# Kernel tuning notes

Hardware: AMD Instinct MI355X
Metric: run time of the kernel (lower is better)

Reference implementation:

```python
import jax, jax.numpy as jnp
import numpy as np

RATIO, NH, NG, KS, RF, UP = 4, 2, 2, 3, 11.0, 2


def _cln(t, g, b):
    # channel-wise LayerNorm on NCHW (LayerNormProxy), eps=1e-5
    mu = t.mean(axis=1, keepdims=True)
    var = ((t - mu) ** 2).mean(axis=1, keepdims=True)
    return (t - mu) * jax.lax.rsqrt(var + 1e-5) * g[None, :, None, None] + b[None, :, None, None]


def _resize_ac(img, oH, oW):
    # bilinear resize, align_corners=True (F.interpolate)
    H, W = img.shape[-2], img.shape[-1]
    ys = jnp.arange(oH, dtype=img.dtype) * ((H - 1) / (oH - 1))
    y0 = jnp.clip(jnp.floor(ys), 0, H - 2).astype(jnp.int32)
    wy = ys - y0.astype(img.dtype)
    xs = jnp.arange(oW, dtype=img.dtype) * ((W - 1) / (oW - 1))
    x0 = jnp.clip(jnp.floor(xs), 0, W - 2).astype(jnp.int32)
    wx = xs - x0.astype(img.dtype)
    t = img[..., y0, :] * (1.0 - wy)[:, None] + img[..., y0 + 1, :] * wy[:, None]
    return t[..., x0] * (1.0 - wx) + t[..., x0 + 1] * wx


def _grid_sample(img, iy, ix):
    # bilinear grid_sample, padding_mode='zeros', align_corners=True
    # img [Bg,Cx,H,W]; iy,ix [Bg,N] unnormalized input-pixel coords
    H, W = img.shape[-2], img.shape[-1]
    def one(im, yy, xx):
        y0f, x0f = jnp.floor(yy), jnp.floor(xx)
        wy, wx = yy - y0f, xx - x0f
        y0, x0 = y0f.astype(jnp.int32), x0f.astype(jnp.int32)
        def gat(yi, xi):
            valid = ((yi >= 0) & (yi < H) & (xi >= 0) & (xi < W)).astype(im.dtype)
            return im[:, jnp.clip(yi, 0, H - 1), jnp.clip(xi, 0, W - 1)] * valid[None]
        return (gat(y0, x0) * ((1 - wy) * (1 - wx))[None]
                + gat(y0, x0 + 1) * ((1 - wy) * wx)[None]
                + gat(y0 + 1, x0) * (wy * (1 - wx))[None]
                + gat(y0 + 1, x0 + 1) * (wy * wx)[None])
    return jax.vmap(one)(img, iy, ix)


def _conv2d(x, w, groups=1):
    return jax.lax.conv_general_dilated(x, w, (1, 1), 'SAME', feature_group_count=groups,
                                        dimension_numbers=('NCHW', 'OIHW', 'NCHW'))


def _forward(x, ln_g, ln_b, Wq, Wk, dw_w, off_ln_g, off_ln_b, off_w, off_b, rpb):
    B, C, H, W = x.shape
    hidden = C // RATIO
    gc = hidden // NG
    c2 = hidden // NH          # attn_dim per head
    oH, oW = int(H * UP), int(W * UP)
    N1, n = oH * oW, KS * KS
    scale = c2 ** -0.5
    v = x
    xn = _cln(x, ln_g, ln_b)
    q = jnp.einsum('oc,bchw->bohw', Wq, xn)
    k = jnp.einsum('oc,bchw->bohw', Wk, xn)
    q = _resize_ac(q, oH, oW)                        # [B,hidden,oH,oW]
    # offset prediction
    q_off = q.reshape(B * NG, gc, oH, oW)
    t = _conv2d(q_off, dw_w, groups=gc)
    t = _cln(t, off_ln_g, off_ln_b)
    t = jax.nn.gelu(t, approximate=False)
    pred = _conv2d(t, off_w) + off_b[None, :, None, None]  # [Bg,2*ks^2,oH,oW]
    pad = (KS - 1) // 2
    rng = jnp.arange(-pad, pad + 1, dtype=x.dtype)
    base = jnp.stack(jnp.meshgrid(rng, rng, indexing='ij'), axis=-1)  # [KS,KS,2] (y,x)
    off = jnp.tanh(pred).reshape(B * NG, KS, KS, 2, oH, oW) * RF + base[None, :, :, :, None, None]
    py = off[:, :, :, 0] + jnp.arange(oH, dtype=x.dtype)[None, None, None, :, None]
    px = off[:, :, :, 1] + jnp.arange(oW, dtype=x.dtype)[None, None, None, None, :]
    # normalize over (oH-1,oW-1) then denormalize onto (H-1,W-1) input grid (align_corners)
    iy = (py * ((H - 1) / (oH - 1))).reshape(B * NG, -1)
    ix = (px * ((W - 1) / (oW - 1))).reshape(B * NG, -1)
    kg = k.reshape(B * NG, hidden // NG, H, W)
    vg = v.reshape(B * NG, C // NG, H, W)
    kf = _grid_sample(kg, iy, ix).reshape(B, NG, hidden // NG, n, oH, oW)
    vf = _grid_sample(vg, iy, ix).reshape(B, NG, C // NG, n, oH, oW)
    # -> [B, N1, n, g*c] -> [B, nh, N1, n, c]
    kf = kf.transpose(0, 4, 5, 3, 1, 2).reshape(B, N1, n, NH, hidden // NH).transpose(0, 3, 1, 2, 4)
    vf = vf.transpose(0, 4, 5, 3, 1, 2).reshape(B, N1, n, NH, C // NH).transpose(0, 3, 1, 2, 4)
    kf = kf + rpb                                     # relative position bias on K
    qh = q.reshape(B, NH, c2, N1).transpose(0, 1, 3, 2) * scale  # [B,nh,N1,c2]
    attn = jax.nn.softmax(jnp.einsum('bhnc,bhnkc->bhnk', qh, kf), axis=-1)
    out = jnp.einsum('bhnk,bhnkc->bhnc', attn, vf)    # [B,nh,N1,C/nh]
    return out.transpose(0, 1, 3, 2).reshape(B, C, oH, oW)


def setup_inputs() -> dict:
    key = jax.random.key(0)
    ks = jax.random.split(key, 8)
    B, C, H, W = 2, 256, 48, 48
    hidden = C // RATIO
    gc = hidden // NG
    c2 = hidden // NH
    f32 = jnp.float32
    return {
        'x': jax.random.normal(ks[0], (B, C, H, W), f32),
        'ln_g': jnp.ones((C,), f32),
        'ln_b': jnp.zeros((C,), f32),
        'Wq': jax.random.normal(ks[1], (hidden, C), f32) * 0.05,
        'Wk': jax.random.normal(ks[2], (hidden, C), f32) * 0.05,
        'dw_w': jax.random.normal(ks[3], (gc, 1, 3, 3), f32) * 0.1,
        'off_ln_g': jnp.ones((gc,), f32),
        'off_ln_b': jnp.zeros((gc,), f32),
        'off_w': jax.random.normal(ks[4], (2 * KS * KS, gc, 3, 3), f32) * 0.02,
        'off_b': jnp.zeros((2 * KS * KS,), f32),
        'rpb': jax.random.normal(ks[5], (1, NH, 1, KS * KS, c2), f32) * 0.02,
    }


def reference(x, ln_g, ln_b, Wq, Wk, dw_w, off_ln_g, off_ln_b, off_w, off_b, rpb):
    return _forward(x, ln_g, ln_b, Wq, Wk, dw_w, off_ln_g, off_ln_b, off_w, off_b, rpb)
```

## Files before the change

### kernel.cpp

```cpp
#include <hip/hip_runtime.h>
#include <cstdint>
#include <cmath>

#define NB 2
#define NC 256
#define HW 2304
#define HID 64
#define OH 96
#define OW 96
#define N1 9216
#define SCALE_ATTN 0.17677669529663689f
#define RESZ ((float)(47.0/95.0))

__device__ __host__ inline int ocb_of(int w) { return w < 2 ? w * 5 : 10 + (w - 2) * 4; }
__device__ __host__ inline int cnt_of(int w) { return w < 2 ? 5 : 4; }

__global__ void kA_prep(const float* __restrict__ Wq, const float* __restrict__ Wk,
                        const float* __restrict__ off_w, const float* __restrict__ dw_w,
                        const float* __restrict__ off_b,
                        float* __restrict__ WT4, float* __restrict__ dwT,
                        float* __restrict__ wg, float* __restrict__ bsg) {
    int idx = blockIdx.x * 256 + threadIdx.x;
    if (idx < 256 * 128) {
        int c = idx >> 7, t = idx & 127;
        float v = (t < 64) ? Wq[t * 256 + c] : Wk[(t - 64) * 256 + c];
        WT4[(((size_t)(c >> 2) * 128) + t) * 4 + (c & 3)] = v;
    } else if (idx < 256 * 128 + 288) {
        int i = idx - 256 * 128;
        int wi = i >> 5, c = i & 31;
        dwT[i] = dw_w[c * 9 + wi];
    } else if (idx < 256 * 128 + 288 + 4 * 288 * 5) {
        int i = idx - (256 * 128 + 288);
        int w = i / 1440, r = i - w * 1440;
        int kk = r / 5, j = r - kk * 5;
        wg[i] = (j < cnt_of(w)) ? off_w[(ocb_of(w) + j) * 288 + kk] : 0.f;
    } else if (idx < 256 * 128 + 288 + 4 * 288 * 5 + 20) {
        int i = idx - (256 * 128 + 288 + 4 * 288 * 5);
        int w = i / 5, j = i - w * 5;
        bsg[i] = (j < cnt_of(w)) ? off_b[ocb_of(w) + j] : 0.f;
    }
}

__global__ __launch_bounds__(256) void k1_ln_qk(const float* __restrict__ x,
                         const float* __restrict__ ln_g, const float* __restrict__ ln_b,
                         const float* __restrict__ WT4,
                         float* __restrict__ q_pix, float* __restrict__ k_nhwc) {
    int blk = blockIdx.x;
    int tid = threadIdx.x;
    int wv = tid >> 6, lane = tid & 63;
    __shared__ float xs[4][256];
    {
        int pix = blk * 4 + wv;
        int b = pix / HW, p = pix - b * HW;
        const float* xb = x + (size_t)b * NC * HW + p;
        float v0 = xb[(size_t)lane * HW];
        float v1 = xb[(size_t)(lane + 64) * HW];
        float v2 = xb[(size_t)(lane + 128) * HW];
        float v3 = xb[(size_t)(lane + 192) * HW];
        float s = v0 + v1 + v2 + v3;
#pragma unroll
        for (int off = 1; off < 64; off <<= 1) s += __shfl_xor(s, off);
        float mu = s * (1.f / 256.f);
        float d0 = v0 - mu, d1 = v1 - mu, d2 = v2 - mu, d3 = v3 - mu;
        float q = d0 * d0 + d1 * d1 + d2 * d2 + d3 * d3;
#pragma unroll
        for (int off = 1; off < 64; off <<= 1) q += __shfl_xor(q, off);
        float rs = rsqrtf(q * (1.f / 256.f) + 1e-5f);
        xs[wv][lane]       = d0 * rs * ln_g[lane]       + ln_b[lane];
        xs[wv][lane + 64]  = d1 * rs * ln_g[lane + 64]  + ln_b[lane + 64];
        xs[wv][lane + 128] = d2 * rs * ln_g[lane + 128] + ln_b[lane + 128];
        xs[wv][lane + 192] = d3 * rs * ln_g[lane + 192] + ln_b[lane + 192];
    }
    __syncthreads();
    int o = tid & 127, ph = tid >> 7;
    float a0 = 0.f, a1 = 0.f;
    const float4* wp = (const float4*)WT4 + o;
    const float4* xa = (const float4*)xs[ph * 2];
    const float4* xb4 = (const float4*)xs[ph * 2 + 1];
#pragma unroll 8
    for (int c4 = 0; c4 < 64; c4++) {
        float4 w = wp[(size_t)c4 * 128];
        float4 p0 = xa[c4], p1 = xb4[c4];
        a0 += w.x * p0.x + w.y * p0.y + w.z * p0.z + w.w * p0.w;
        a1 += w.x * p1.x + w.y * p1.y + w.z * p1.z + w.w * p1.w;
    }
#pragma unroll
    for (int k = 0; k < 2; k++) {
        int pix = blk * 4 + ph * 2 + k;
        int b = pix / HW, p = pix - b * HW;
        float a = k ? a1 : a0;
        if (o < 64) {
            q_pix[(((size_t)b * HW) + p) * 64 + o] = a;
        } else {
            int t = o - 64, g = t >> 5, c32 = t & 31;
            k_nhwc[(((size_t)(b * 2 + g) * HW) + p) * 32 + c32] = a;
        }
    }
}

__global__ __launch_bounds__(256) void k3_t(const float* __restrict__ q_pix,
                                            const float* __restrict__ dwT,
                                            const float* __restrict__ og,
                                            const float* __restrict__ ob,
                                            float* __restrict__ tbuf) {
    int gid = blockIdx.x * 256 + threadIdx.x;
    int c = gid & 31;
    int p2 = gid >> 5;
    int bg = p2 / N1, p = p2 - bg * N1;
    int b = bg >> 1, g = bg & 1;
    int oy = p / OW, ox = p - oy * OW;
    const float* qb = q_pix + ((size_t)b * HW) * 64 + g * 32 + c;
    float acc = 0.f;
#pragma unroll
    for (int dy = -1; dy <= 1; dy++) {
        int yy = oy + dy;
        if ((unsigned)yy >= (unsigned)OH) continue;
        float ysf = yy * RESZ;
        int y0 = min((int)ysf, 46);
        float wy = ysf - (float)y0;
#pragma unroll
        for (int dx = -1; dx <= 1; dx++) {
            int xx = ox + dx;
            if ((unsigned)xx >= (unsigned)OW) continue;
            float xsf = xx * RESZ;
            int x0 = min((int)xsf, 46);
            float wx = xsf - (float)x0;
            int i00 = (y0 * 48 + x0) * 64;
            float q00 = qb[i00], q01 = qb[i00 + 64];
            float q10 = qb[i00 + 48 * 64], q11 = qb[i00 + 49 * 64];
            float qv = (q00 * (1.f - wy) + q10 * wy) * (1.f - wx)
                     + (q01 * (1.f - wy) + q11 * wy) * wx;
            acc += qv * dwT[((dy + 1) * 3 + dx + 1) * 32 + c];
        }
    }
    float s = acc;
#pragma unroll
    for (int off = 1; off < 32; off <<= 1) s += __shfl_xor(s, off);
    float mu = s * (1.f / 32.f);
    float d = acc - mu;
    float v = d * d;
#pragma unroll
    for (int off = 1; off < 32; off <<= 1) v += __shfl_xor(v, off);
    float rsv = rsqrtf(v * (1.f / 32.f) + 1e-5f);
    float t = d * rsv * og[c] + ob[c];
    float ge = 0.5f * t * (1.f + erff(t * 0.70710678118654752f));
    tbuf[(size_t)p2 * 32 + c] = ge;
}

__global__ __launch_bounds__(256) void k4_pred(const float* __restrict__ tbuf,
                                               const float* __restrict__ wg,
                                               const float* __restrict__ bsg,
                                               float* __restrict__ pred) {
    int blk = blockIdx.x;
    int bg = blk / 144, tile = blk - bg * 144;
    int ty0 = (tile / 12) * 8, tx0 = (tile % 12) * 8;
    int tid = threadIdx.x;
    __shared__ float ts[100 * 33];

    const float* tb = tbuf + (size_t)bg * N1 * 32;
    for (int item = tid; item < 800; item += 256) {
        int pt = item >> 3, q = item & 7;
        int hy = ty0 + pt / 10 - 1;
        int hx = tx0 + pt % 10 - 1;
        float4 v = make_float4(0.f, 0.f, 0.f, 0.f);
        if ((unsigned)hy < (unsigned)OH && (unsigned)hx < (unsigned)OW)
            v = *(const float4*)(tb + ((size_t)(hy * OW + hx)) * 32 + q * 4);
        int base = pt * 33 + q * 4;
        ts[base] = v.x; ts[base + 1] = v.y; ts[base + 2] = v.z; ts[base + 3] = v.w;
    }
    __syncthreads();

    int w = __builtin_amdgcn_readfirstlane(tid >> 6);
    int lane = tid & 63;
    int y = lane >> 3, x = lane & 7;
    int ocb = ocb_of(w), cnt = cnt_of(w);
    float acc[5];
#pragma unroll
    for (int j = 0; j < 5; j++) acc[j] = bsg[w * 5 + j];
    const float* tsb = &ts[(y * 10 + x) * 33];
    const float* wgp = wg + (size_t)w * 1440;
    const int kof[9] = {0, 33, 66, 330, 363, 396, 660, 693, 726};
    for (int ic = 0; ic < 32; ic++) {
#pragma unroll
        for (int k = 0; k < 9; k++) {
            float tv = tsb[kof[k] + ic];
            const float* wr = wgp + (ic * 9 + k) * 5;
#pragma unroll
            for (int j = 0; j < 5; j++) acc[j] += tv * wr[j];
        }
    }
    int p = (ty0 + y) * OW + tx0 + x;
    float* pp = pred + ((size_t)bg * N1 + p) * 18 + ocb;
#pragma unroll
    for (int j = 0; j < 5; j++)
        if (j < cnt) pp[j] = acc[j];
}

__global__ void k2b_vt(const float* __restrict__ x, float* __restrict__ v_nhwc) {
    int blk = blockIdx.x;
    int pt = blk % 72;
    int t2 = blk / 72;
    int ct = t2 & 3;
    int bg = t2 >> 2;
    int b = bg >> 1, g = bg & 1;
    __shared__ float tile[32][33];
    int tx = threadIdx.x & 31, row = threadIdx.x >> 5;
#pragma unroll
    for (int r = 0; r < 4; r++) {
        int c = ct * 32 + row + r * 8;
        tile[row + r * 8][tx] = x[((size_t)(b * 256 + g * 128 + c)) * HW + pt * 32 + tx];
    }
    __syncthreads();
#pragma unroll
    for (int r = 0; r < 4; r++) {
        int p = pt * 32 + row + r * 8;
        v_nhwc[((size_t)bg * HW + p) * 128 + ct * 32 + tx] = tile[tx][row + r * 8];
    }
}

__global__ __launch_bounds__(256) void k5_attn(const float* __restrict__ pred,
                                               const float* __restrict__ q_pix,
                                               const float* __restrict__ k_nhwc,
                                               const float* __restrict__ v_nhwc,
                                               const float* __restrict__ rpb,
                                               float* __restrict__ out) {
    int tid = threadIdx.x;
    int wv = __builtin_amdgcn_readfirstlane(tid >> 6);
    int lane = tid & 63;
    int gp = blockIdx.x * 16;
    int bg = gp / N1, p0 = gp % N1;
    int b = bg >> 1, g = bg & 1;
    int pw = p0 + wv * 4;
    int oy = pw / OW, ox0 = pw % OW;

    __shared__ float4 wts[4][4][9];
    __shared__ int4   cof[4][4][9];
    __shared__ float  outb[4][4][128];

    if (lane < 36) {
        int px = lane / 9, j = lane % 9;
        int p = pw + px;
        int ky = j / 3, kx = j % 3;
        const float* pp = pred + ((size_t)bg * N1 + p) * 18;
        float pr0 = pp[j * 2];
        float pr1 = pp[j * 2 + 1];
        float th0 = 1.f - 2.f * __builtin_amdgcn_rcpf(__expf(2.f * pr0) + 1.f);
        float th1 = 1.f - 2.f * __builtin_amdgcn_rcpf(__expf(2.f * pr1) + 1.f);
        float py  = th0 * 11.0f + (float)(ky - 1) + (float)oy;
        float pxc = th1 * 11.0f + (float)(kx - 1) + (float)(ox0 + px);
        float iy = py * RESZ, ix = pxc * RESZ;
        float y0f = floorf(iy), x0f = floorf(ix);
        float wy = iy - y0f, wx = ix - x0f;
        int y0 = (int)y0f, x0 = (int)x0f;
        bool vy0 = (unsigned)y0 < 48u, vy1 = (unsigned)(y0 + 1) < 48u;
        bool vx0 = (unsigned)x0 < 48u, vx1 = (unsigned)(x0 + 1) < 48u;
        int y0c = min(max(y0, 0), 47), y1c = min(max(y0 + 1, 0), 47);
        int x0c = min(max(x0, 0), 47), x1c = min(max(x0 + 1, 0), 47);
        float4 w;
        w.x = (vy0 && vx0) ? (1.f - wy) * (1.f - wx) : 0.f;
        w.y = (vy0 && vx1) ? (1.f - wy) * wx : 0.f;
        w.z = (vy1 && vx0) ? wy * (1.f - wx) : 0.f;
        w.w = (vy1 && vx1) ? wy * wx : 0.f;
        wts[wv][px][j] = w;
        cof[wv][px][j] = make_int4(y0c * 48 + x0c, y0c * 48 + x1c,
                                   y1c * 48 + x0c, y1c * 48 + x1c);
    }
    __syncthreads();

    int c = lane & 31, h = lane >> 5;
    int c4 = (lane & 31) * 4;
    const float* kb = k_nhwc + (size_t)bg * HW * 32;
    const float* rb = rpb + (size_t)g * 288;
    const float* qb = q_pix + (size_t)b * HW * 64 + g * 32 + c;
    const float* vbase = v_nhwc + (size_t)bg * HW * 128;

    float ysf = oy * RESZ;
    int qy0 = min((int)ysf, 46);
    float qwy = ysf - (float)qy0;

    for (int px = 0; px < 4; px++) {
        float xsf = (ox0 + px) * RESZ;
        int qx0 = min((int)xsf, 46);
        float qwx = xsf - (float)qx0;
        int qi = (qy0 * 48 + qx0) * 64;
        float q00 = qb[qi], q01 = qb[qi + 64];
        float q10 = qb[qi + 48 * 64], q11 = qb[qi + 49 * 64];
        float qv = ((q00 * (1.f - qwy) + q10 * qwy) * (1.f - qwx)
                  + (q01 * (1.f - qwy) + q11 * qwy) * qwx) * SCALE_ATTN;

        float s[5], e[5];
#pragma unroll
        for (int jj = 0; jj < 5; jj++) {
            int j = jj * 2 + h;
            float partial = 0.f;
            if (j < 9) {
                float4 w = wts[wv][px][j];
                int4 co = cof[wv][px][j];
                float kv = w.x * kb[co.x * 32 + c] + w.y * kb[co.y * 32 + c]
                         + w.z * kb[co.z * 32 + c] + w.w * kb[co.w * 32 + c];
                partial = qv * (kv + rb[j * 32 + c]);
            }
#pragma unroll
            for (int off = 1; off < 32; off <<= 1) partial += __shfl_xor(partial, off);
            s[jj] = (j < 9) ? partial : -1e30f;
        }
        float m = s[0];
#pragma unroll
        for (int jj = 1; jj < 5; jj++) m = fmaxf(m, s[jj]);
        m = fmaxf(m, __shfl_xor(m, 32));
        float sum = 0.f;
#pragma unroll
        for (int jj = 0; jj < 5; jj++) { e[jj] = __expf(s[jj] - m); sum += e[jj]; }
        sum += __shfl_xor(sum, 32);
        float inv = __builtin_amdgcn_rcpf(sum);

        float4 acc = make_float4(0.f, 0.f, 0.f, 0.f);
#pragma unroll
        for (int jj = 0; jj < 5; jj++) {
            int j = jj * 2 + h;
            if (j < 9) {
                float pj = e[jj] * inv;
                float4 w = wts[wv][px][j];
                int4 co = cof[wv][px][j];
                float4 a0 = *(const float4*)(vbase + (size_t)co.x * 128 + c4);
                float4 a1 = *(const float4*)(vbase + (size_t)co.y * 128 + c4);
                float4 a2 = *(const float4*)(vbase + (size_t)co.z * 128 + c4);
                float4 a3 = *(const float4*)(vbase + (size_t)co.w * 128 + c4);
                float f0 = w.x * pj, f1 = w.y * pj, f2 = w.z * pj, f3 = w.w * pj;
                acc.x += f0 * a0.x + f1 * a1.x + f2 * a2.x + f3 * a3.x;
                acc.y += f0 * a0.y + f1 * a1.y + f2 * a2.y + f3 * a3.y;
                acc.z += f0 * a0.z + f1 * a1.z + f2 * a2.z + f3 * a3.z;
                acc.w += f0 * a0.w + f1 * a1.w + f2 * a2.w + f3 * a3.w;
            }
        }
        acc.x += __shfl_xor(acc.x, 32);
        acc.y += __shfl_xor(acc.y, 32);
        acc.z += __shfl_xor(acc.z, 32);
        acc.w += __shfl_xor(acc.w, 32);
        if (lane < 32) *(float4*)&outb[wv][px][c4] = acc;
    }
    __syncthreads();

    if (tid < 128) {
        int ch = tid;
        float* op = out + ((size_t)b * NC + g * 128 + ch) * N1 + p0;
#pragma unroll
        for (int w2 = 0; w2 < 4; w2++) {
            float4 v4 = make_float4(outb[w2][0][ch], outb[w2][1][ch],
                                    outb[w2][2][ch], outb[w2][3][ch]);
            *(float4*)(op + w2 * 4) = v4;
        }
    }
}

extern "C" void kernel_launch(void* const* d_in, const int* in_sizes, int n_in,
                              void* d_out, int out_size, void* d_ws, size_t ws_size,
                              hipStream_t stream) {
    const float* x      = (const float*)d_in[0];
    const float* ln_g   = (const float*)d_in[1];
    const float* ln_b   = (const float*)d_in[2];
    const float* Wq     = (const float*)d_in[3];
    const float* Wk     = (const float*)d_in[4];
    const float* dw_w   = (const float*)d_in[5];
    const float* off_g  = (const float*)d_in[6];
    const float* off_bt = (const float*)d_in[7];
    const float* off_w  = (const float*)d_in[8];
    const float* off_b  = (const float*)d_in[9];
    const float* rpb    = (const float*)d_in[10];
    float* out = (float*)d_out;

    float* ws = (float*)d_ws;
    float* U      = ws;
    float* tbuf   = U;
    float* v_nhwc = U;
    float* WT4    = U + 1179648;
    float* k_nhwc = WT4 + 32768;
    float* q_pix  = k_nhwc + 294912;
    float* pred   = q_pix + 294912;
    float* dwT    = pred + 663552;
    float* wg     = dwT + 288;
    float* bsg    = wg + 5760;

    kA_prep<<<173, 256, 0, stream>>>(Wq, Wk, off_w, dw_w, off_b, WT4, dwT, wg, bsg);
    k1_ln_qk<<<1152, 256, 0, stream>>>(x, ln_g, ln_b, WT4, q_pix, k_nhwc);
    k3_t<<<4608, 256, 0, stream>>>(q_pix, dwT, off_g, off_bt, tbuf);
    k4_pred<<<576, 256, 0, stream>>>(tbuf, wg, bsg, pred);
    k2b_vt<<<1152, 256, 0, stream>>>(x, v_nhwc);
    k5_attn<<<2304, 256, 0, stream>>>(pred, q_pix, k_nhwc, v_nhwc, rpb, out);
}
```

Measured before the change: 175.7 us.

## Fuse depthwise/LN/GELU into offset conv and merge V transpose into prep

Merges the x→NHWC transpose into the weight-prep kernel so k1 reads the contiguous NHWC copy instead of strided NCHW. The depthwise-conv, layernorm and GELU stage is fused into the offset-prediction kernel, so each tile computes its halo directly from q_pix and tbuf is never written to or read back from global memory. This cuts two launches and one large intermediate buffer. The cost is recomputing the halo entries and having k1 depend on the transpose finishing first.

Result: slower. 185.1 us (+5.3%).

```diff
diff --git a/kernel.cpp b/kernel.cpp
--- a/kernel.cpp
+++ b/kernel.cpp
@@ -15,33 +15,56 @@
 __device__ __host__ inline int ocb_of(int w) { return w < 2 ? w * 5 : 10 + (w - 2) * 4; }
 __device__ __host__ inline int cnt_of(int w) { return w < 2 ? 5 : 4; }
 
-__global__ void kA_prep(const float* __restrict__ Wq, const float* __restrict__ Wk,
-                        const float* __restrict__ off_w, const float* __restrict__ dw_w,
-                        const float* __restrict__ off_b,
-                        float* __restrict__ WT4, float* __restrict__ dwT,
-                        float* __restrict__ wg, float* __restrict__ bsg) {
-    int idx = blockIdx.x * 256 + threadIdx.x;
-    if (idx < 256 * 128) {
-        int c = idx >> 7, t = idx & 127;
-        float v = (t < 64) ? Wq[t * 256 + c] : Wk[(t - 64) * 256 + c];
-        WT4[(((size_t)(c >> 2) * 128) + t) * 4 + (c & 3)] = v;
-    } else if (idx < 256 * 128 + 288) {
-        int i = idx - 256 * 128;
-        int wi = i >> 5, c = i & 31;
-        dwT[i] = dw_w[c * 9 + wi];
-    } else if (idx < 256 * 128 + 288 + 4 * 288 * 5) {
-        int i = idx - (256 * 128 + 288);
-        int w = i / 1440, r = i - w * 1440;
-        int kk = r / 5, j = r - kk * 5;
-        wg[i] = (j < cnt_of(w)) ? off_w[(ocb_of(w) + j) * 288 + kk] : 0.f;
-    } else if (idx < 256 * 128 + 288 + 4 * 288 * 5 + 20) {
-        int i = idx - (256 * 128 + 288 + 4 * 288 * 5);
-        int w = i / 5, j = i - w * 5;
-        bsg[i] = (j < cnt_of(w)) ? off_b[ocb_of(w) + j] : 0.f;
-    }
-}
-
-__global__ __launch_bounds__(256) void k1_ln_qk(const float* __restrict__ x,
+__global__ void kA_prep(const float* __restrict__ x, const float* __restrict__ Wq,
+                        const float* __restrict__ Wk, const float* __restrict__ off_w,
+                        const float* __restrict__ dw_w, const float* __restrict__ off_b,
+                        float* __restrict__ v_nhwc, float* __restrict__ WT4,
+                        float* __restrict__ dwT, float* __restrict__ wg,
+                        float* __restrict__ bsg) {
+    int blk = blockIdx.x;
+    if (blk < 1152) {
+        int pt = blk % 72;
+        int t2 = blk / 72;
+        int ct = t2 & 3;
+        int bg = t2 >> 2;
+        int b = bg >> 1, g = bg & 1;
+        __shared__ float tile[32][33];
+        int tx = threadIdx.x & 31, row = threadIdx.x >> 5;
+#pragma unroll
+        for (int r = 0; r < 4; r++) {
+            int c = ct * 32 + row + r * 8;
+            tile[row + r * 8][tx] = x[((size_t)(b * 256 + g * 128 + c)) * HW + pt * 32 + tx];
+        }
+        __syncthreads();
+#pragma unroll
+        for (int r = 0; r < 4; r++) {
+            int p = pt * 32 + row + r * 8;
+            v_nhwc[((size_t)bg * HW + p) * 128 + ct * 32 + tx] = tile[tx][row + r * 8];
+        }
+    } else {
+        int idx = (blk - 1152) * 256 + threadIdx.x;
+        if (idx < 256 * 128) {
+            int c = idx >> 7, t = idx & 127;
+            float v = (t < 64) ? Wq[t * 256 + c] : Wk[(t - 64) * 256 + c];
+            WT4[(((size_t)(c >> 2) * 128) + t) * 4 + (c & 3)] = v;
+        } else if (idx < 256 * 128 + 288) {
+            int i = idx - 256 * 128;
+            int wi = i >> 5, c = i & 31;
+            dwT[i] = dw_w[c * 9 + wi];
+        } else if (idx < 256 * 128 + 288 + 4 * 288 * 5) {
+            int i = idx - (256 * 128 + 288);
+            int w = i / 1440, r = i - w * 1440;
+            int kk = r / 5, j = r - kk * 5;
+            wg[i] = (j < cnt_of(w)) ? off_w[(ocb_of(w) + j) * 288 + kk] : 0.f;
+        } else if (idx < 256 * 128 + 288 + 4 * 288 * 5 + 20) {
+            int i = idx - (256 * 128 + 288 + 4 * 288 * 5);
+            int w = i / 5, j = i - w * 5;
+            bsg[i] = (j < cnt_of(w)) ? off_b[ocb_of(w) + j] : 0.f;
+        }
+    }
+}
+
+__global__ __launch_bounds__(256) void k1_ln_qk(const float* __restrict__ v_nhwc,
                          const float* __restrict__ ln_g, const float* __restrict__ ln_b,
                          const float* __restrict__ WT4,
                          float* __restrict__ q_pix, float* __restrict__ k_nhwc) {
@@ -52,24 +75,25 @@
     {
         int pix = blk * 4 + wv;
         int b = pix / HW, p = pix - b * HW;
-        const float* xb = x + (size_t)b * NC * HW + p;
-        float v0 = xb[(size_t)lane * HW];
-        float v1 = xb[(size_t)(lane + 64) * HW];
-        float v2 = xb[(size_t)(lane + 128) * HW];
-        float v3 = xb[(size_t)(lane + 192) * HW];
-        float s = v0 + v1 + v2 + v3;
+        int c0 = lane * 2;
+        float2 u0 = *(const float2*)(v_nhwc + (((size_t)(b * 2 + 0) * HW) + p) * 128 + c0);
+        float2 u1 = *(const float2*)(v_nhwc + (((size_t)(b * 2 + 1) * HW) + p) * 128 + c0);
+        float s = u0.x + u0.y + u1.x + u1.y;
 #pragma unroll
         for (int off = 1; off < 64; off <<= 1) s += __shfl_xor(s, off);
         float mu = s * (1.f / 256.f);
-        float d0 = v0 - mu, d1 = v1 - mu, d2 = v2 - mu, d3 = v3 - mu;
+        float d0 = u0.x - mu, d1 = u0.y - mu, d2 = u1.x - mu, d3 = u1.y - mu;
         float q = d0 * d0 + d1 * d1 + d2 * d2 + d3 * d3;
 #pragma unroll
         for (int off = 1; off < 64; off <<= 1) q += __shfl_xor(q, off);
         float rs = rsqrtf(q * (1.f / 256.f) + 1e-5f);
-        xs[wv][lane]       = d0 * rs * ln_g[lane]       + ln_b[lane];
-        xs[wv][lane + 64]  = d1 * rs * ln_g[lane + 64]  + ln_b[lane + 64];
-        xs[wv][lane + 128] = d2 * rs * ln_g[lane + 128] + ln_b[lane + 128];
-        xs[wv][lane + 192] = d3 * rs * ln_g[lane + 192] + ln_b[lane + 192];
+        float2 w0, w1;
+        w0.x = d0 * rs * ln_g[c0] + ln_b[c0];
+        w0.y = d1 * rs * ln_g[c0 + 1] + ln_b[c0 + 1];
+        w1.x = d2 * rs * ln_g[128 + c0] + ln_b[128 + c0];
+        w1.y = d3 * rs * ln_g[129 + c0] + ln_b[129 + c0];
+        *(float2*)&xs[wv][c0] = w0;
+        *(float2*)&xs[wv][128 + c0] = w1;
     }
     __syncthreads();
     int o = tid & 127, ph = tid >> 7;
@@ -98,75 +122,63 @@
     }
 }
 
-__global__ __launch_bounds__(256) void k3_t(const float* __restrict__ q_pix,
-                                            const float* __restrict__ dwT,
-                                            const float* __restrict__ og,
-                                            const float* __restrict__ ob,
-                                            float* __restrict__ tbuf) {
-    int gid = blockIdx.x * 256 + threadIdx.x;
-    int c = gid & 31;
-    int p2 = gid >> 5;
-    int bg = p2 / N1, p = p2 - bg * N1;
-    int b = bg >> 1, g = bg & 1;
-    int oy = p / OW, ox = p - oy * OW;
-    const float* qb = q_pix + ((size_t)b * HW) * 64 + g * 32 + c;
-    float acc = 0.f;
-#pragma unroll
-    for (int dy = -1; dy <= 1; dy++) {
-        int yy = oy + dy;
-        if ((unsigned)yy >= (unsigned)OH) continue;
-        float ysf = yy * RESZ;
-        int y0 = min((int)ysf, 46);
-        float wy = ysf - (float)y0;
-#pragma unroll
-        for (int dx = -1; dx <= 1; dx++) {
-            int xx = ox + dx;
-            if ((unsigned)xx >= (unsigned)OW) continue;
-            float xsf = xx * RESZ;
-            int x0 = min((int)xsf, 46);
-            float wx = xsf - (float)x0;
-            int i00 = (y0 * 48 + x0) * 64;
-            float q00 = qb[i00], q01 = qb[i00 + 64];
-            float q10 = qb[i00 + 48 * 64], q11 = qb[i00 + 49 * 64];
-            float qv = (q00 * (1.f - wy) + q10 * wy) * (1.f - wx)
-                     + (q01 * (1.f - wy) + q11 * wy) * wx;
-            acc += qv * dwT[((dy + 1) * 3 + dx + 1) * 32 + c];
-        }
-    }
-    float s = acc;
-#pragma unroll
-    for (int off = 1; off < 32; off <<= 1) s += __shfl_xor(s, off);
-    float mu = s * (1.f / 32.f);
-    float d = acc - mu;
-    float v = d * d;
-#pragma unroll
-    for (int off = 1; off < 32; off <<= 1) v += __shfl_xor(v, off);
-    float rsv = rsqrtf(v * (1.f / 32.f) + 1e-5f);
-    float t = d * rsv * og[c] + ob[c];
-    float ge = 0.5f * t * (1.f + erff(t * 0.70710678118654752f));
-    tbuf[(size_t)p2 * 32 + c] = ge;
-}
-
-__global__ __launch_bounds__(256) void k4_pred(const float* __restrict__ tbuf,
+__global__ __launch_bounds__(256) void k34_off(const float* __restrict__ q_pix,
+                                               const float* __restrict__ dwT,
+                                               const float* __restrict__ og,
+                                               const float* __restrict__ ob,
                                                const float* __restrict__ wg,
                                                const float* __restrict__ bsg,
                                                float* __restrict__ pred) {
     int blk = blockIdx.x;
     int bg = blk / 144, tile = blk - bg * 144;
     int ty0 = (tile / 12) * 8, tx0 = (tile % 12) * 8;
+    int b = bg >> 1, g = bg & 1;
     int tid = threadIdx.x;
     __shared__ float ts[100 * 33];
 
-    const float* tb = tbuf + (size_t)bg * N1 * 32;
-    for (int item = tid; item < 800; item += 256) {
-        int pt = item >> 3, q = item & 7;
-        int hy = ty0 + pt / 10 - 1;
-        int hx = tx0 + pt % 10 - 1;
-        float4 v = make_float4(0.f, 0.f, 0.f, 0.f);
-        if ((unsigned)hy < (unsigned)OH && (unsigned)hx < (unsigned)OW)
-            v = *(const float4*)(tb + ((size_t)(hy * OW + hx)) * 32 + q * 4);
-        int base = pt * 33 + q * 4;
-        ts[base] = v.x; ts[base + 1] = v.y; ts[base + 2] = v.z; ts[base + 3] = v.w;
+    const float* qb = q_pix + ((size_t)b * HW) * 64 + g * 32;
+    for (int item = tid; item < 3200; item += 256) {
+        int pt = item >> 5, c = item & 31;
+        int pyh = pt / 10, pxh = pt - pyh * 10;
+        int hy = ty0 + pyh - 1, hx = tx0 + pxh - 1;
+        bool inb = ((unsigned)hy < (unsigned)OH) && ((unsigned)hx < (unsigned)OW);
+        float acc = 0.f;
+        if (inb) {
+#pragma unroll
+            for (int dy = -1; dy <= 1; dy++) {
+                int yy = hy + dy;
+                if ((unsigned)yy >= (unsigned)OH) continue;
+                float ysf = yy * RESZ;
+                int y0 = min((int)ysf, 46);
+                float wy = ysf - (float)y0;
+#pragma unroll
+                for (int dx = -1; dx <= 1; dx++) {
+                    int xx = hx + dx;
+                    if ((unsigned)xx >= (unsigned)OW) continue;
+                    float xsf = xx * RESZ;
+                    int x0 = min((int)xsf, 46);
+                    float wx = xsf - (float)x0;
+                    int i00 = (y0 * 48 + x0) * 64;
+                    float q00 = qb[i00 + c], q01 = qb[i00 + 64 + c];
+                    float q10 = qb[i00 + 48 * 64 + c], q11 = qb[i00 + 49 * 64 + c];
+                    float qv = (q00 * (1.f - wy) + q10 * wy) * (1.f - wx)
+                             + (q01 * (1.f - wy) + q11 * wy) * wx;
+                    acc += qv * dwT[((dy + 1) * 3 + dx + 1) * 32 + c];
+                }
+            }
+        }
+        float s = acc;
+#pragma unroll
+        for (int off = 1; off < 32; off <<= 1) s += __shfl_xor(s, off);
+        float mu = s * (1.f / 32.f);
+        float d = acc - mu;
+        float v = d * d;
+#pragma unroll
+        for (int off = 1; off < 32; off <<= 1) v += __shfl_xor(v, off);
+        float rsv = rsqrtf(v * (1.f / 32.f) + 1e-5f);
+        float t = d * rsv * og[c] + ob[c];
+        float ge = 0.5f * t * (1.f + erff(t * 0.70710678118654752f));
+        ts[pt * 33 + c] = inb ? ge : 0.f;
     }
     __syncthreads();
 
@@ -194,28 +206,6 @@
 #pragma unroll
     for (int j = 0; j < 5; j++)
         if (j < cnt) pp[j] = acc[j];
-}
-
-__global__ void k2b_vt(const float* __restrict__ x, float* __restrict__ v_nhwc) {
-    int blk = blockIdx.x;
-    int pt = blk % 72;
-    int t2 = blk / 72;
-    int ct = t2 & 3;
-    int bg = t2 >> 2;
-    int b = bg >> 1, g = bg & 1;
-    __shared__ float tile[32][33];
-    int tx = threadIdx.x & 31, row = threadIdx.x >> 5;
-#pragma unroll
-    for (int r = 0; r < 4; r++) {
-        int c = ct * 32 + row + r * 8;
-        tile[row + r * 8][tx] = x[((size_t)(b * 256 + g * 128 + c)) * HW + pt * 32 + tx];
-    }
-    __syncthreads();
-#pragma unroll
-    for (int r = 0; r < 4; r++) {
-        int p = pt * 32 + row + r * 8;
-        v_nhwc[((size_t)bg * HW + p) * 128 + ct * 32 + tx] = tile[tx][row + r * 8];
-    }
 }
 
 __global__ __launch_bounds__(256) void k5_attn(const float* __restrict__ pred,
@@ -370,10 +360,8 @@
     float* out = (float*)d_out;
 
     float* ws = (float*)d_ws;
-    float* U      = ws;
-    float* tbuf   = U;
-    float* v_nhwc = U;
-    float* WT4    = U + 1179648;
+    float* v_nhwc = ws;
+    float* WT4    = v_nhwc + 1179648;
     float* k_nhwc = WT4 + 32768;
     float* q_pix  = k_nhwc + 294912;
     float* pred   = q_pix + 294912;
@@ -381,10 +369,9 @@
     float* wg     = dwT + 288;
     float* bsg    = wg + 5760;
 
-    kA_prep<<<173, 256, 0, stream>>>(Wq, Wk, off_w, dw_w, off_b, WT4, dwT, wg, bsg);
-    k1_ln_qk<<<1152, 256, 0, stream>>>(x, ln_g, ln_b, WT4, q_pix, k_nhwc);
-    k3_t<<<4608, 256, 0, stream>>>(q_pix, dwT, off_g, off_bt, tbuf);
-    k4_pred<<<576, 256, 0, stream>>>(tbuf, wg, bsg, pred);
-    k2b_vt<<<1152, 256, 0, stream>>>(x, v_nhwc);
+    kA_prep<<<1304, 256, 0, stream>>>(x, Wq, Wk, off_w, dw_w, off_b,
+                                      v_nhwc, WT4, dwT, wg, bsg);
+    k1_ln_qk<<<1152, 256, 0, stream>>>(v_nhwc, ln_g, ln_b, WT4, q_pix, k_nhwc);
+    k34_off<<<576, 256, 0, stream>>>(q_pix, dwT, off_g, off_bt, wg, bsg, pred);
     k5_attn<<<2304, 256, 0, stream>>>(pred, q_pix, k_nhwc, v_nhwc, rpb, out);
 }
```
